# Optimization experiments

Hardware: AMD Instinct MI355X
Metric: run time of the kernel (lower is better)

## Reference

```python
import jax, jax.numpy as jnp
import numpy as np

K, S = 8, 4  # patch kernel and stride (overlapping: stride < kernel)


def _patch_idx(H, W):
    nH = (H - K) // S + 1
    nW = (W - K) // S + 1
    hh = (jnp.arange(nH) * S)[:, None] + jnp.arange(K)[None, :]  # [nH, K]
    ww = (jnp.arange(nW) * S)[:, None] + jnp.arange(K)[None, :]  # [nW, K]
    return nH, nW, hh, ww


def _split(x):
    # x: [B, C, H, W] -> [B*N, K*K, C] (same token/patch ordering as nn.Unfold)
    B, C, H, W = x.shape
    nH, nW, hh, ww = _patch_idx(H, W)
    # gather overlapping patches: [B, C, nH, nW, K, K]
    p = x[:, :, hh[:, None, :, None], ww[None, :, None, :]]
    p = jnp.transpose(p, (0, 2, 3, 4, 5, 1))  # [B, nH, nW, K, K, C]
    return p.reshape(B * nH * nW, K * K, C)


def _merge(z, B, C, H, W):
    # z: [B*N, K*K, C] -> overlap-add fold -> [B, C, H, W] (matches nn.Fold)
    nH, nW, hh, ww = _patch_idx(H, W)
    y = z.reshape(B, nH, nW, K, K, C)
    y = jnp.transpose(y, (0, 5, 1, 2, 3, 4))  # [B, C, nH, nW, K, K]
    out = jnp.zeros((B, C, H, W), z.dtype)
    out = out.at[:, :, hh[:, None, :, None], ww[None, :, None, :]].add(y)
    return out


def reference(q, k, v):
    B, C, H, W = v.shape
    qp = _split(q)  # [BN, KK, C]
    kp = _split(k)
    vp = _split(v)
    scale = C ** (-0.5)
    # per-patch attention over KK=64 tokens
    attn = jax.nn.softmax(scale * jnp.einsum('ntc,nsc->nts', qp, kp), axis=-1)
    z = jnp.einsum('nts,nsc->ntc', attn, vp)  # [BN, KK, C]
    return _merge(z, B, C, H, W)


def setup_inputs() -> dict:
    key = jax.random.key(0)
    k1, k2, k3 = jax.random.split(key, 3)
    shape = (8, 128, 128, 128)  # [B, C, H, W]
    return {
        'q': jax.random.normal(k1, shape, dtype=jnp.float32),
        'k': jax.random.normal(k2, shape, dtype=jnp.float32),
        'v': jax.random.normal(k3, shape, dtype=jnp.float32),
    }
```

## Files before the change

### kernel.cpp

```cpp
#include <hip/hip_runtime.h>

#define B_    8
#define C_    128
#define H_    128
#define W_    128
#define NH    31
#define NPB   (NH*NH)
#define NPAT  (B_*NPB)
#define HW_   (H_*W_)
#define CHW_  (C_*HW_)
#define WS_BYTES ((size_t)NPAT * 8192 * 2)

typedef float v4f __attribute__((ext_vector_type(4)));
typedef short v8s __attribute__((ext_vector_type(8)));

__device__ __forceinline__ unsigned short f2bf(float f) {
    unsigned int u = __builtin_bit_cast(unsigned int, f);
    u += 0x7FFFu + ((u >> 16) & 1u);
    return (unsigned short)(u >> 16);
}
__device__ __forceinline__ unsigned int pack2bf(float lo, float hi) {
    return (unsigned int)f2bf(lo) | ((unsigned int)f2bf(hi) << 16);
}
__device__ __forceinline__ float bflo(unsigned int d) {
    return __builtin_bit_cast(float, d << 16);
}
__device__ __forceinline__ float bfhi(unsigned int d) {
    return __builtin_bit_cast(float, d & 0xFFFF0000u);
}


__global__ __launch_bounds__(256, 4)
void patch_attn_ws(const float* __restrict__ q,
                   const float* __restrict__ k,
                   const float* __restrict__ v,
                   unsigned short* __restrict__ ws)
{
    __shared__ __align__(16) unsigned char lds[32768];
    unsigned short* sQ  = (unsigned short*)(lds);
    unsigned short* sK  = (unsigned short*)(lds + 16384);
    unsigned short* sVT = (unsigned short*)(lds);
    unsigned short* sP  = (unsigned short*)(lds + 16384);
    unsigned short* sRep= (unsigned short*)(lds);

    const int tid  = threadIdx.x;
    const int lane = tid & 63;
    const int l15  = lane & 15;
    const int quad = lane >> 4;
    const int wid  = tid >> 6;

    const int p   = (blockIdx.x & 7) * NPB + (blockIdx.x >> 3);
    const int b   = p / NPB;
    const int rem = p - b * NPB;
    const int ph  = rem / NH;
    const int pw  = rem - ph * NH;
    const int h0  = ph * 4, w0 = pw * 4;
    const int baseB = b * CHW_;

    {
        float4 qa[4], qb[4], ka[4], kb[4];
        int c0A[4], tA[4];
        #pragma unroll
        for (int g = 0; g < 4; ++g) {
            int flat2 = tid + g * 256;
            int jj = flat2 & 1;
            int i  = (flat2 >> 1) & 7;
            int cp = flat2 >> 4;
            int c0 = cp * 2;
            int off0 = baseB + c0 * HW_ + (h0 + i) * W_ + (w0 + jj * 4);
            qa[g] = *(const float4*)(q + off0);
            qb[g] = *(const float4*)(q + off0 + HW_);
            ka[g] = *(const float4*)(k + off0);
            kb[g] = *(const float4*)(k + off0 + HW_);
            c0A[g] = c0;
            tA[g]  = i * 8 + jj * 4;
        }
        #pragma unroll
        for (int g = 0; g < 4; ++g) {
            const float* fqa = (const float*)&qa[g];
            const float* fqb = (const float*)&qb[g];
            const float* fka = (const float*)&ka[g];
            const float* fkb = (const float*)&kb[g];
            int c0 = c0A[g];
            #pragma unroll
            for (int d = 0; d < 4; ++d) {
                int t = tA[g] + d;
                int chunk = (c0 >> 3) ^ (t & 15);
                int pos = t * 128 + chunk * 8 + (c0 & 7);
                *(unsigned int*)&sQ[pos] = pack2bf(fqa[d], fqb[d]);
                *(unsigned int*)&sK[pos] = pack2bf(fka[d], fkb[d]);
            }
        }
    }
    __syncthreads();

    v4f acc0, acc1, acc2, acc3;
    acc0 = acc1 = acc2 = acc3 = (v4f){0.f, 0.f, 0.f, 0.f};
    const int rowT = wid * 16 + l15;
    #pragma unroll
    for (int kk = 0; kk < 4; ++kk) {
        int gph = (kk * 4 + quad) ^ l15;
        v8s bq = *(const v8s*)(&sQ[rowT * 128 + gph * 8]);
        v8s a0 = *(const v8s*)(&sK[( 0 + l15) * 128 + gph * 8]);
        v8s a1 = *(const v8s*)(&sK[(16 + l15) * 128 + gph * 8]);
        v8s a2 = *(const v8s*)(&sK[(32 + l15) * 128 + gph * 8]);
        v8s a3 = *(const v8s*)(&sK[(48 + l15) * 128 + gph * 8]);
        acc0 = __builtin_amdgcn_mfma_f32_16x16x32_bf16(a0, bq, acc0, 0, 0, 0);
        acc1 = __builtin_amdgcn_mfma_f32_16x16x32_bf16(a1, bq, acc1, 0, 0, 0);
        acc2 = __builtin_amdgcn_mfma_f32_16x16x32_bf16(a2, bq, acc2, 0, 0, 0);
        acc3 = __builtin_amdgcn_mfma_f32_16x16x32_bf16(a3, bq, acc3, 0, 0, 0);
    }

    float4 rv[8];
    int cV[8], sV[8];
    #pragma unroll
    for (int g = 0; g < 8; ++g) {
        int flat4 = tid + g * 256;
        int jj = flat4 & 1;
        int i  = (flat4 >> 1) & 7;
        int c  = flat4 >> 4;
        rv[g] = *(const float4*)(v + baseB + c * HW_ + (h0 + i) * W_ + (w0 + jj * 4));
        cV[g] = c;
        sV[g] = i * 8 + jj * 4;
    }

    const float scale = 0.08838834764831845f;
    float e0[4], e1[4], e2[4], e3[4];
    unsigned int pPk[8];
    {
        float mx = -1e30f;
        #pragma unroll
        for (int r = 0; r < 4; ++r) {
            e0[r] = acc0[r] * scale; mx = fmaxf(mx, e0[r]);
            e1[r] = acc1[r] * scale; mx = fmaxf(mx, e1[r]);
            e2[r] = acc2[r] * scale; mx = fmaxf(mx, e2[r]);
            e3[r] = acc3[r] * scale; mx = fmaxf(mx, e3[r]);
        }
        mx = fmaxf(mx, __shfl_xor(mx, 16));
        mx = fmaxf(mx, __shfl_xor(mx, 32));
        float sum = 0.f;
        #pragma unroll
        for (int r = 0; r < 4; ++r) {
            e0[r] = __expf(e0[r] - mx); sum += e0[r];
            e1[r] = __expf(e1[r] - mx); sum += e1[r];
            e2[r] = __expf(e2[r] - mx); sum += e2[r];
            e3[r] = __expf(e3[r] - mx); sum += e3[r];
        }
        sum += __shfl_xor(sum, 16);
        sum += __shfl_xor(sum, 32);
        float inv = 1.0f / sum;
        pPk[0] = pack2bf(e0[0] * inv, e0[1] * inv);
        pPk[1] = pack2bf(e0[2] * inv, e0[3] * inv);
        pPk[2] = pack2bf(e1[0] * inv, e1[1] * inv);
        pPk[3] = pack2bf(e1[2] * inv, e1[3] * inv);
        pPk[4] = pack2bf(e2[0] * inv, e2[1] * inv);
        pPk[5] = pack2bf(e2[2] * inv, e2[3] * inv);
        pPk[6] = pack2bf(e3[0] * inv, e3[1] * inv);
        pPk[7] = pack2bf(e3[2] * inv, e3[3] * inv);
    }
    __syncthreads();

    #pragma unroll
    for (int g = 0; g < 8; ++g) {
        const float* fv = (const float*)&rv[g];
        int c = cV[g], s0 = sV[g];
        unsigned int w0p = pack2bf(fv[0], fv[1]);
        unsigned int w1p = pack2bf(fv[2], fv[3]);
        int idx = c * 64 + ((((s0 >> 3) ^ (c & 7)) << 3) | (s0 & 7));
        uint2 val; val.x = w0p; val.y = w1p;
        *(uint2*)(&sVT[idx]) = val;
    }

    {
        const int t = rowT;
        const int qh = quad >> 1, ql = quad & 1;
        #pragma unroll
        for (int m = 0; m < 4; ++m) {
            int chunk = (m * 2 + qh) ^ (t & 7);
            uint2 val;
            val.x = pPk[m * 2];
            val.y = pPk[m * 2 + 1];
            *(uint2*)(&sP[t * 64 + chunk * 8 + ql * 4]) = val;
        }
    }
    __syncthreads();

    v4f z00, z01, z02, z03, z10, z11, z12, z13;
    z00 = z01 = z02 = z03 = (v4f){0.f, 0.f, 0.f, 0.f};
    z10 = z11 = z12 = z13 = (v4f){0.f, 0.f, 0.f, 0.f};
    #pragma unroll
    for (int kk = 0; kk < 2; ++kk) {
        int gph = (kk * 4 + quad) ^ (l15 & 7);
        v8s b0 = *(const v8s*)(&sP[( 0 + l15) * 64 + gph * 8]);
        v8s b1 = *(const v8s*)(&sP[(16 + l15) * 64 + gph * 8]);
        v8s b2 = *(const v8s*)(&sP[(32 + l15) * 64 + gph * 8]);
        v8s b3 = *(const v8s*)(&sP[(48 + l15) * 64 + gph * 8]);
        v8s aA = *(const v8s*)(&sVT[(wid * 32      + l15) * 64 + gph * 8]);
        v8s aB = *(const v8s*)(&sVT[(wid * 32 + 16 + l15) * 64 + gph * 8]);
        z00 = __builtin_amdgcn_mfma_f32_16x16x32_bf16(aA, b0, z00, 0, 0, 0);
        z01 = __builtin_amdgcn_mfma_f32_16x16x32_bf16(aA, b1, z01, 0, 0, 0);
        z02 = __builtin_amdgcn_mfma_f32_16x16x32_bf16(aA, b2, z02, 0, 0, 0);
        z03 = __builtin_amdgcn_mfma_f32_16x16x32_bf16(aA, b3, z03, 0, 0, 0);
        z10 = __builtin_amdgcn_mfma_f32_16x16x32_bf16(aB, b0, z10, 0, 0, 0);
        z11 = __builtin_amdgcn_mfma_f32_16x16x32_bf16(aB, b1, z11, 0, 0, 0);
        z12 = __builtin_amdgcn_mfma_f32_16x16x32_bf16(aB, b2, z12, 0, 0, 0);
        z13 = __builtin_amdgcn_mfma_f32_16x16x32_bf16(aB, b3, z13, 0, 0, 0);
    }
    __syncthreads();

    {
        const int cb0 = wid * 32 + quad * 4;
        #pragma unroll
        for (int r = 0; r < 4; ++r) {
            int cA = cb0 + r, cB = cb0 + 16 + r;
            sRep[cA * 66 + ( 0 + l15)] = f2bf(z00[r]);
            sRep[cA * 66 + (16 + l15)] = f2bf(z01[r]);
            sRep[cA * 66 + (32 + l15)] = f2bf(z02[r]);
            sRep[cA * 66 + (48 + l15)] = f2bf(z03[r]);
            sRep[cB * 66 + ( 0 + l15)] = f2bf(z10[r]);
            sRep[cB * 66 + (16 + l15)] = f2bf(z11[r]);
            sRep[cB * 66 + (32 + l15)] = f2bf(z12[r]);
            sRep[cB * 66 + (48 + l15)] = f2bf(z13[r]);
        }
    }
    __syncthreads();

    {
        int c = tid >> 1, th = tid & 1;
        const unsigned short* src = &sRep[c * 66 + th * 32];
        uint2 d0 = *(const uint2*)(src);
        uint2 d1 = *(const uint2*)(src + 4);
        uint2 d2 = *(const uint2*)(src + 8);
        uint2 d3 = *(const uint2*)(src + 12);
        uint2 d4 = *(const uint2*)(src + 16);
        uint2 d5 = *(const uint2*)(src + 20);
        uint2 d6 = *(const uint2*)(src + 24);
        uint2 d7 = *(const uint2*)(src + 28);
        unsigned short* dst = ws + (size_t)p * 8192 + c * 64 + th * 32;
        uint4 w0v; w0v.x = d0.x; w0v.y = d0.y; w0v.z = d1.x; w0v.w = d1.y;
        uint4 w1v; w1v.x = d2.x; w1v.y = d2.y; w1v.z = d3.x; w1v.w = d3.y;
        uint4 w2v; w2v.x = d4.x; w2v.y = d4.y; w2v.z = d5.x; w2v.w = d5.y;
        uint4 w3v; w3v.x = d6.x; w3v.y = d6.y; w3v.z = d7.x; w3v.w = d7.y;
        ((uint4*)dst)[0] = w0v;
        ((uint4*)dst)[1] = w1v;
        ((uint4*)dst)[2] = w2v;
        ((uint4*)dst)[3] = w3v;
    }
}


#define MSLOT 264
#define MARR  (33 * MSLOT)

__global__ __launch_bounds__(256, 4)
void merge_kernel(const unsigned short* __restrict__ ws,
                  float* __restrict__ out)
{
    __shared__ __align__(16) unsigned short sM[2 * MARR];
    unsigned short* sA = sM;
    unsigned short* sB = sM + MARR;

    const int tid  = threadIdx.x;
    const int b    = blockIdx.x & 7;
    const int rest = blockIdx.x >> 3;
    const int hq   = rest >> 4;
    const int cg   = rest & 15;

    if (tid < 132) {
        int target = tid / 33;
        int j      = tid - target * 33;
        unsigned short* base = ((target < 2) ? sA : sB)
                             + ((target & 1) ? 32 * MSLOT : 0);
        uint4 zz; zz.x = 0u; zz.y = 0u; zz.z = 0u; zz.w = 0u;
        *(uint4*)(base + j * 8) = zz;
    }

    const int aValid = (hq <= 30);
    const int bValid = (hq >= 1);
    const int hqB = bValid ? (hq - 1) : 0;
    const size_t rowA = (size_t)(b * NPB + hq  * NH) * 8192;
    const size_t rowB = (size_t)(b * NPB + hqB * NH) * 8192;

    #pragma unroll
    for (int it = 0; it < 8; ++it) {
        int flat = tid + it * 256;
        if (flat < 1984) {
            int half = (flat >= 992);
            int fl   = flat - (half ? 992 : 0);
            int seg  = fl >> 2;
            int sub  = fl & 3;
            int pw   = seg >> 3;
            int csub = seg & 7;
            const unsigned short* src = ws
                + (half ? rowB : rowA)
                + (size_t)pw * 8192
                + (size_t)(cg * 8 + csub) * 64
                + (half ? 32 : 0)
                + sub * 8;
            int valid = half ? bValid : aValid;
            uint4 val;
            if (valid) {
                val = *(const uint4*)src;
            } else {
                val.x = 0u; val.y = 0u; val.z = 0u; val.w = 0u;
            }
            unsigned short* dst = (half ? sB : sA)
                + (pw + 1) * MSLOT + csub * 32 + sub * 8;
            *(uint4*)dst = val;
        }
    }
    __syncthreads();

    const int l    = tid & 31;
    const int csub = tid >> 5;
    const int c    = cg * 8 + csub;

    float* op = out + b * CHW_ + c * HW_ + (hq * 4) * W_ + l * 4;
    #pragma unroll
    for (int hr = 0; hr < 4; ++hr) {
        int baseL = (l + 1) * MSLOT + csub * 32 + hr * 8;
        int baseP = l       * MSLOT + csub * 32 + hr * 8 + 4;
        uint2 aL = *(const uint2*)(sA + baseL);
        uint2 aP = *(const uint2*)(sA + baseP);
        uint2 bL = *(const uint2*)(sB + baseL);
        uint2 bP = *(const uint2*)(sB + baseP);
        float4 r;
        r.x = bflo(aL.x) + bflo(aP.x) + bflo(bL.x) + bflo(bP.x);
        r.y = bfhi(aL.x) + bfhi(aP.x) + bfhi(bL.x) + bfhi(bP.x);
        r.z = bflo(aL.y) + bflo(aP.y) + bflo(bL.y) + bflo(bP.y);
        r.w = bfhi(aL.y) + bfhi(aP.y) + bfhi(bL.y) + bfhi(bP.y);
        *(float4*)(op + hr * W_) = r;
    }
}


__global__ __launch_bounds__(512, 6)
void patch_attn_atomic(const float* __restrict__ q,
                       const float* __restrict__ k,
                       const float* __restrict__ v,
                       float* __restrict__ out)
{
    __shared__ __align__(16) unsigned char lds[43264];
    unsigned short* sQ   = (unsigned short*)(lds);
    unsigned short* sK   = (unsigned short*)(lds + 16384);
    unsigned short* sVT  = (unsigned short*)(lds);
    unsigned short* sP   = (unsigned short*)(lds + 32768);
    float*          sRedM= (float*)(lds + 40960);
    float*          sRedL= (float*)(lds + 41984);
    float*          sInv = (float*)(lds + 43008);

    const int tid  = threadIdx.x;
    const int lane = tid & 63;
    const int wid  = tid >> 6;
    const int l15  = lane & 15;
    const int quad = lane >> 4;

    const int p   = (blockIdx.x & 7) * NPB + (blockIdx.x >> 3);
    const int b   = p / NPB;
    const int rem = p - b * NPB;
    const int ph  = rem / NH;
    const int pw  = rem - ph * NH;
    const int h0  = ph * 4, w0 = pw * 4;
    const int baseB = b * CHW_;

    float4 rq[4], rk[4], rv[4];
    int cA[4], tA[4];
    #pragma unroll
    for (int g = 0; g < 4; ++g) {
        int flat4 = tid + g * 512;
        int jj = flat4 & 1;
        int i  = (flat4 >> 1) & 7;
        int c  = flat4 >> 4;
        int off = baseB + c * HW_ + (h0 + i) * W_ + (w0 + jj * 4);
        rq[g] = *(const float4*)(q + off);
        rk[g] = *(const float4*)(k + off);
        rv[g] = *(const float4*)(v + off);
        cA[g] = c;
        tA[g] = i * 8 + jj * 4;
    }
    #pragma unroll
    for (int g = 0; g < 4; ++g) {
        const float* fq = (const float*)&rq[g];
        const float* fk = (const float*)&rk[g];
        int c = cA[g];
        #pragma unroll
        for (int d = 0; d < 4; ++d) {
            int t = tA[g] + d;
            int idx = t * 128 + ((((c >> 3) ^ (t & 15)) << 3) | (c & 7));
            sQ[idx] = f2bf(fq[d]);
            sK[idx] = f2bf(fk[d]);
        }
    }
    __syncthreads();

    const float scale = 0.08838834764831845f;
    const int nt  = wid & 3;
    const int mt0 = wid >> 2;

    v4f accT[2];
    #pragma unroll
    for (int ti = 0; ti < 2; ++ti) {
        int mt = mt0 + ti * 2;
        v4f acc = {0.f, 0.f, 0.f, 0.f};
        int rowA = mt * 16 + l15;
        int rowB = nt * 16 + l15;
        #pragma unroll
        for (int kk = 0; kk < 4; ++kk) {
            int gph = (kk * 4 + quad) ^ l15;
            v8s a  = *(const v8s*)(&sQ[rowA * 128 + gph * 8]);
            v8s bb = *(const v8s*)(&sK[rowB * 128 + gph * 8]);
            acc = __builtin_amdgcn_mfma_f32_16x16x32_bf16(a, bb, acc, 0, 0, 0);
        }
        #pragma unroll
        for (int r = 0; r < 4; ++r) acc[r] *= scale;
        accT[ti] = acc;
    }

    float4 mloc[2], eV[2];
    #pragma unroll
    for (int ti = 0; ti < 2; ++ti) {
        float4 m;
        #pragma unroll
        for (int r = 0; r < 4; ++r) m[r] = accT[ti][r];
        #pragma unroll
        for (int mask = 1; mask <= 8; mask <<= 1)
            #pragma unroll
            for (int r = 0; r < 4; ++r) m[r] = fmaxf(m[r], __shfl_xor(m[r], mask));
        float4 e, l;
        #pragma unroll
        for (int r = 0; r < 4; ++r) { e[r] = __expf(accT[ti][r] - m[r]); l[r] = e[r]; }
        #pragma unroll
        for (int mask = 1; mask <= 8; mask <<= 1)
            #pragma unroll
            for (int r = 0; r < 4; ++r) l[r] += __shfl_xor(l[r], mask);
        mloc[ti] = m; eV[ti] = e;
        if (l15 == 0) {
            int tb = (mt0 + ti * 2) * 16 + quad * 4;
            #pragma unroll
            for (int r = 0; r < 4; ++r) {
                sRedM[nt * 64 + tb + r] = m[r];
                sRedL[nt * 64 + tb + r] = l[r];
            }
        }
    }
    __syncthreads();

    #pragma unroll
    for (int g = 0; g < 4; ++g) {
        const float* fv = (const float*)&rv[g];
        unsigned short tmp[4];
        #pragma unroll
        for (int d = 0; d < 4; ++d) tmp[d] = f2bf(fv[d]);
        int c = cA[g], s0 = tA[g];
        int idx = c * 64 + ((((s0 >> 3) ^ (c & 7)) << 3) | (s0 & 7));
        *(uint2*)(&sVT[idx]) = *(const uint2*)tmp;
    }

    #pragma unroll
    for (int ti = 0; ti < 2; ++ti) {
        int tb = (mt0 + ti * 2) * 16 + quad * 4;
        float4 Mv[4], Lv[4];
        #pragma unroll
        for (int n2 = 0; n2 < 4; ++n2) {
            Mv[n2] = *(const float4*)(&sRedM[n2 * 64 + tb]);
            Lv[n2] = *(const float4*)(&sRedL[n2 * 64 + tb]);
        }
        float4 M = Mv[0], L;
        #pragma unroll
        for (int n2 = 1; n2 < 4; ++n2)
            #pragma unroll
            for (int r = 0; r < 4; ++r) M[r] = fmaxf(M[r], Mv[n2][r]);
        #pragma unroll
        for (int r = 0; r < 4; ++r) L[r] = 0.f;
        #pragma unroll
        for (int n2 = 0; n2 < 4; ++n2)
            #pragma unroll
            for (int r = 0; r < 4; ++r) L[r] += Lv[n2][r] * __expf(Mv[n2][r] - M[r]);
        #pragma unroll
        for (int r = 0; r < 4; ++r) {
            float pv = eV[ti][r] * __expf(mloc[ti][r] - M[r]);
            int t = tb + r;
            int s = nt * 16 + l15;
            sP[t * 64 + ((((s >> 3) ^ (t & 7)) << 3) | (s & 7))] = f2bf(pv);
        }
        if (nt == 0 && l15 == 0) {
            #pragma unroll
            for (int r = 0; r < 4; ++r) sInv[tb + r] = 1.0f / L[r];
        }
    }
    __syncthreads();

    v4f z[4];
    #pragma unroll
    for (int n2 = 0; n2 < 4; ++n2) z[n2] = (v4f){0.f, 0.f, 0.f, 0.f};
    const int crow = wid * 16 + l15;
    #pragma unroll
    for (int kk = 0; kk < 2; ++kk) {
        int gph = (kk * 4 + quad) ^ (l15 & 7);
        v8s a = *(const v8s*)(&sVT[crow * 64 + gph * 8]);
        #pragma unroll
        for (int n2 = 0; n2 < 4; ++n2) {
            int trow = n2 * 16 + l15;
            v8s bb = *(const v8s*)(&sP[trow * 64 + gph * 8]);
            z[n2] = __builtin_amdgcn_mfma_f32_16x16x32_bf16(a, bb, z[n2], 0, 0, 0);
        }
    }

    #pragma unroll
    for (int n2 = 0; n2 < 4; ++n2) {
        int t = n2 * 16 + l15;
        float inv = sInv[t];
        int base2 = baseB + (h0 + (t >> 3)) * W_ + (w0 + (t & 7));
        #pragma unroll
        for (int r = 0; r < 4; ++r) {
            int c = wid * 16 + quad * 4 + r;
            unsafeAtomicAdd(out + base2 + c * HW_, z[n2][r] * inv);
        }
    }
}

extern "C" void kernel_launch(void* const* d_in, const int* in_sizes, int n_in,
                              void* d_out, int out_size, void* d_ws, size_t ws_size,
                              hipStream_t stream) {
    const float* q = (const float*)d_in[0];
    const float* k = (const float*)d_in[1];
    const float* v = (const float*)d_in[2];
    float* out = (float*)d_out;

    if (ws_size >= WS_BYTES) {
        unsigned short* ws = (unsigned short*)d_ws;
        patch_attn_ws<<<NPAT, 256, 0, stream>>>(q, k, v, ws);
        merge_kernel<<<8 * 32 * 16, 256, 0, stream>>>(ws, out);
    } else {
        hipMemsetAsync(out, 0, (size_t)out_size * sizeof(float), stream);
        patch_attn_atomic<<<NPAT, 512, 0, stream>>>(q, k, v, out);
    }
}
```

Measured before the change: 347.4 us.

## Store workspace token-major directly from MFMA registers, skipping LDS transpose

The attention kernel now writes its bf16 output straight from the MFMA accumulators into a token-major workspace layout ([token][channel]). A permuted channel-row mapping (rA) puts each lane's four accumulator values on adjacent channels, so they pack into one 16-byte store. This removes the LDS staging buffer and two block barriers. The merge kernel's gather and sum indexing is changed to match the new layout, trading vector LDS reads for scalar 16-bit reads, and the attention kernel's launch-bounds occupancy hint is raised from 4 to 5.

```diff
diff --git a/kernel.cpp b/kernel.cpp
--- a/kernel.cpp
+++ b/kernel.cpp
@@ -22,15 +22,12 @@
 __device__ __forceinline__ unsigned int pack2bf(float lo, float hi) {
     return (unsigned int)f2bf(lo) | ((unsigned int)f2bf(hi) << 16);
 }
-__device__ __forceinline__ float bflo(unsigned int d) {
-    return __builtin_bit_cast(float, d << 16);
-}
-__device__ __forceinline__ float bfhi(unsigned int d) {
-    return __builtin_bit_cast(float, d & 0xFFFF0000u);
-}
-
-
-__global__ __launch_bounds__(256, 4)
+__device__ __forceinline__ float bfs(unsigned short u) {
+    return __builtin_bit_cast(float, ((unsigned int)u) << 16);
+}
+
+
+__global__ __launch_bounds__(256, 5)
 void patch_attn_ws(const float* __restrict__ q,
                    const float* __restrict__ k,
                    const float* __restrict__ v,
@@ -41,7 +38,6 @@
     unsigned short* sK  = (unsigned short*)(lds + 16384);
     unsigned short* sVT = (unsigned short*)(lds);
     unsigned short* sP  = (unsigned short*)(lds + 16384);
-    unsigned short* sRep= (unsigned short*)(lds);
 
     const int tid  = threadIdx.x;
     const int lane = tid & 63;
@@ -164,9 +160,10 @@
     for (int g = 0; g < 8; ++g) {
         const float* fv = (const float*)&rv[g];
         int c = cV[g], s0 = sV[g];
+        int kV = (c & 3) | (((c >> 3) & 1) << 2);
         unsigned int w0p = pack2bf(fv[0], fv[1]);
         unsigned int w1p = pack2bf(fv[2], fv[3]);
-        int idx = c * 64 + ((((s0 >> 3) ^ (c & 7)) << 3) | (s0 & 7));
+        int idx = c * 64 + ((((s0 >> 3) ^ kV) << 3) | (s0 & 7));
         uint2 val; val.x = w0p; val.y = w1p;
         *(uint2*)(&sVT[idx]) = val;
     }
@@ -188,6 +185,8 @@
     v4f z00, z01, z02, z03, z10, z11, z12, z13;
     z00 = z01 = z02 = z03 = (v4f){0.f, 0.f, 0.f, 0.f};
     z10 = z11 = z12 = z13 = (v4f){0.f, 0.f, 0.f, 0.f};
+    const int wb = wid * 32;
+    const int rA = wb + (l15 & 3) + ((l15 >> 2) << 3);
     #pragma unroll
     for (int kk = 0; kk < 2; ++kk) {
         int gph = (kk * 4 + quad) ^ (l15 & 7);
@@ -195,8 +194,8 @@
         v8s b1 = *(const v8s*)(&sP[(16 + l15) * 64 + gph * 8]);
         v8s b2 = *(const v8s*)(&sP[(32 + l15) * 64 + gph * 8]);
         v8s b3 = *(const v8s*)(&sP[(48 + l15) * 64 + gph * 8]);
-        v8s aA = *(const v8s*)(&sVT[(wid * 32      + l15) * 64 + gph * 8]);
-        v8s aB = *(const v8s*)(&sVT[(wid * 32 + 16 + l15) * 64 + gph * 8]);
+        v8s aA = *(const v8s*)(&sVT[rA * 64 + gph * 8]);
+        v8s aB = *(const v8s*)(&sVT[(rA + 4) * 64 + gph * 8]);
         z00 = __builtin_amdgcn_mfma_f32_16x16x32_bf16(aA, b0, z00, 0, 0, 0);
         z01 = __builtin_amdgcn_mfma_f32_16x16x32_bf16(aA, b1, z01, 0, 0, 0);
         z02 = __builtin_amdgcn_mfma_f32_16x16x32_bf16(aA, b2, z02, 0, 0, 0);
@@ -206,45 +205,27 @@
         z12 = __builtin_amdgcn_mfma_f32_16x16x32_bf16(aB, b2, z12, 0, 0, 0);
         z13 = __builtin_amdgcn_mfma_f32_16x16x32_bf16(aB, b3, z13, 0, 0, 0);
     }
-    __syncthreads();
 
     {
-        const int cb0 = wid * 32 + quad * 4;
-        #pragma unroll
-        for (int r = 0; r < 4; ++r) {
-            int cA = cb0 + r, cB = cb0 + 16 + r;
-            sRep[cA * 66 + ( 0 + l15)] = f2bf(z00[r]);
-            sRep[cA * 66 + (16 + l15)] = f2bf(z01[r]);
-            sRep[cA * 66 + (32 + l15)] = f2bf(z02[r]);
-            sRep[cA * 66 + (48 + l15)] = f2bf(z03[r]);
-            sRep[cB * 66 + ( 0 + l15)] = f2bf(z10[r]);
-            sRep[cB * 66 + (16 + l15)] = f2bf(z11[r]);
-            sRep[cB * 66 + (32 + l15)] = f2bf(z12[r]);
-            sRep[cB * 66 + (48 + l15)] = f2bf(z13[r]);
-        }
-    }
-    __syncthreads();
-
-    {
-        int c = tid >> 1, th = tid & 1;
-        const unsigned short* src = &sRep[c * 66 + th * 32];
-        uint2 d0 = *(const uint2*)(src);
-        uint2 d1 = *(const uint2*)(src + 4);
-        uint2 d2 = *(const uint2*)(src + 8);
-        uint2 d3 = *(const uint2*)(src + 12);
-        uint2 d4 = *(const uint2*)(src + 16);
-        uint2 d5 = *(const uint2*)(src + 20);
-        uint2 d6 = *(const uint2*)(src + 24);
-        uint2 d7 = *(const uint2*)(src + 28);
-        unsigned short* dst = ws + (size_t)p * 8192 + c * 64 + th * 32;
-        uint4 w0v; w0v.x = d0.x; w0v.y = d0.y; w0v.z = d1.x; w0v.w = d1.y;
-        uint4 w1v; w1v.x = d2.x; w1v.y = d2.y; w1v.z = d3.x; w1v.w = d3.y;
-        uint4 w2v; w2v.x = d4.x; w2v.y = d4.y; w2v.z = d5.x; w2v.w = d5.y;
-        uint4 w3v; w3v.x = d6.x; w3v.y = d6.y; w3v.z = d7.x; w3v.w = d7.y;
-        ((uint4*)dst)[0] = w0v;
-        ((uint4*)dst)[1] = w1v;
-        ((uint4*)dst)[2] = w2v;
-        ((uint4*)dst)[3] = w3v;
+        unsigned short* wp = ws + (size_t)p * 8192 + wb + quad * 8;
+        uint4 val;
+        int t;
+        t = 0 + l15;
+        val.x = pack2bf(z00[0], z00[1]); val.y = pack2bf(z00[2], z00[3]);
+        val.z = pack2bf(z10[0], z10[1]); val.w = pack2bf(z10[2], z10[3]);
+        *(uint4*)(wp + t * 128) = val;
+        t = 16 + l15;
+        val.x = pack2bf(z01[0], z01[1]); val.y = pack2bf(z01[2], z01[3]);
+        val.z = pack2bf(z11[0], z11[1]); val.w = pack2bf(z11[2], z11[3]);
+        *(uint4*)(wp + t * 128) = val;
+        t = 32 + l15;
+        val.x = pack2bf(z02[0], z02[1]); val.y = pack2bf(z02[2], z02[3]);
+        val.z = pack2bf(z12[0], z12[1]); val.w = pack2bf(z12[2], z12[3]);
+        *(uint4*)(wp + t * 128) = val;
+        t = 48 + l15;
+        val.x = pack2bf(z03[0], z03[1]); val.y = pack2bf(z03[2], z03[3]);
+        val.z = pack2bf(z13[0], z13[1]); val.w = pack2bf(z13[2], z13[3]);
+        *(uint4*)(wp + t * 128) = val;
     }
 }
 
@@ -287,16 +268,13 @@
         if (flat < 1984) {
             int half = (flat >= 992);
             int fl   = flat - (half ? 992 : 0);
-            int seg  = fl >> 2;
-            int sub  = fl & 3;
-            int pw   = seg >> 3;
-            int csub = seg & 7;
+            int pw   = fl >> 5;
+            int t    = fl & 31;
             const unsigned short* src = ws
                 + (half ? rowB : rowA)
                 + (size_t)pw * 8192
-                + (size_t)(cg * 8 + csub) * 64
-                + (half ? 32 : 0)
-                + sub * 8;
+                + (size_t)(half ? (t + 32) : t) * 128
+                + cg * 8;
             int valid = half ? bValid : aValid;
             uint4 val;
             if (valid) {
@@ -305,7 +283,7 @@
                 val.x = 0u; val.y = 0u; val.z = 0u; val.w = 0u;
             }
             unsigned short* dst = (half ? sB : sA)
-                + (pw + 1) * MSLOT + csub * 32 + sub * 8;
+                + (pw + 1) * MSLOT + t * 8;
             *(uint4*)dst = val;
         }
     }
@@ -315,20 +293,23 @@
     const int csub = tid >> 5;
     const int c    = cg * 8 + csub;
 
+    const int own  = (l + 1) * MSLOT + csub;
+    const int left = l       * MSLOT + csub;
+
     float* op = out + b * CHW_ + c * HW_ + (hq * 4) * W_ + l * 4;
     #pragma unroll
     for (int hr = 0; hr < 4; ++hr) {
-        int baseL = (l + 1) * MSLOT + csub * 32 + hr * 8;
-        int baseP = l       * MSLOT + csub * 32 + hr * 8 + 4;
-        uint2 aL = *(const uint2*)(sA + baseL);
-        uint2 aP = *(const uint2*)(sA + baseP);
-        uint2 bL = *(const uint2*)(sB + baseL);
-        uint2 bP = *(const uint2*)(sB + baseP);
-        float4 r;
-        r.x = bflo(aL.x) + bflo(aP.x) + bflo(bL.x) + bflo(bP.x);
-        r.y = bfhi(aL.x) + bfhi(aP.x) + bfhi(bL.x) + bfhi(bP.x);
-        r.z = bflo(aL.y) + bflo(aP.y) + bflo(bL.y) + bflo(bP.y);
-        r.w = bfhi(aL.y) + bfhi(aP.y) + bfhi(bL.y) + bfhi(bP.y);
+        float rr[4];
+        #pragma unroll
+        for (int j = 0; j < 4; ++j) {
+            int tl = hr * 8 + j;
+            float s = bfs(sA[own  + tl * 8])
+                    + bfs(sA[left + (tl + 4) * 8])
+                    + bfs(sB[own  + tl * 8])
+                    + bfs(sB[left + (tl + 4) * 8]);
+            rr[j] = s;
+        }
+        float4 r; r.x = rr[0]; r.y = rr[1]; r.z = rr[2]; r.w = rr[3];
         *(float4*)(op + hr * W_) = r;
     }
 }
```

New measurement: 363.4 us. 4.6% more time.
